# Performance work log

Measured on AMD Instinct MI355X. Metric: run time of the kernel, lower is better.

## Reference

```python
import jax, jax.numpy as jnp
import numpy as np

B, T, D, R = 4, 2048, 1024, 32


def setup_inputs() -> dict:
    key = jax.random.key(0)
    kx, ku = jax.random.split(key)
    x = jax.random.normal(kx, (B, T, D), dtype=jnp.float32)
    # low-rank metric factor; small init so distances are moderate
    U = jax.random.normal(ku, (D, R), dtype=jnp.float32) * 0.05
    return {"x": x, "U": U}


def reference(x, U):
    # g = U @ U.T (PSD low-rank metric).
    # dist_sq[b,t,j] = (x_t - x_j)^T g (x_t - x_j)
    #               = ||U^T x_t||^2 + ||U^T x_j||^2 - 2 (U^T x_t).(U^T x_j)
    # Algebraic expansion of the original O(B*T*T*D) broadcasted diff tensor.
    y = jnp.einsum('btd,dr->btr', x, U)                # [B,T,R]
    n = jnp.sum(y * y, axis=-1)                         # [B,T]
    cross = jnp.einsum('btr,bjr->btj', y, y)            # [B,T,T]
    dist_sq = n[:, :, None] + n[:, None, :] - 2.0 * cross
    attn = jax.nn.softmax(-dist_sq, axis=-1)            # [B,T,T]
    return jnp.einsum('btj,bjd->btd', attn, x)          # [B,T,D]
```

## Files before the change

### kernel.cpp

```cpp
#include <hip/hip_runtime.h>

#define B_ 4
#define T_ 2048
#define D_ 1024
#define R_ 32
#define XSTR 72

typedef __attribute__((ext_vector_type(8))) short short8;
typedef __attribute__((ext_vector_type(4))) float f32x4;
typedef __attribute__((ext_vector_type(4))) unsigned short us4;
typedef __attribute__((ext_vector_type(8))) unsigned short us8;

__device__ __forceinline__ unsigned short f2bf(float f) {
  union { float f; unsigned u; } v; v.f = f;
  unsigned r = (v.u + 0x7fffu + ((v.u >> 16) & 1u)) >> 16;
  return (unsigned short)r;
}
__device__ __forceinline__ float bf2f(unsigned short h) {
  union { unsigned u; float f; } v; v.u = (unsigned)h << 16;
  return v.f;
}

__global__ __launch_bounds__(256)
void geo_ut(const float* __restrict__ U, unsigned short* __restrict__ Ut) {
  __shared__ float tile[128][33];
  const int tid = threadIdx.x;
  const int d0 = blockIdx.x * 128;
  #pragma unroll
  for (int i = 0; i < 16; i++) {
    int e = i * 256 + tid;
    int d = e >> 5, r = e & 31;
    tile[d][r] = U[(size_t)(d0 + d) * R_ + r];
  }
  __syncthreads();
  const int r = tid >> 3, seg = tid & 7;
  us8 o0, o1;
  #pragma unroll
  for (int k = 0; k < 8; k++) o0[k] = f2bf(tile[seg * 16 + k][r]);
  #pragma unroll
  for (int k = 0; k < 8; k++) o1[k] = f2bf(tile[seg * 16 + 8 + k][r]);
  *(us8*)(Ut + (size_t)r * D_ + d0 + seg * 16) = o0;
  *(us8*)(Ut + (size_t)r * D_ + d0 + seg * 16 + 8) = o1;
}

__global__ __launch_bounds__(256)
void geo_prep(const float* __restrict__ x, const unsigned short* __restrict__ Ut,
              unsigned short* __restrict__ xt, unsigned short* __restrict__ ybf,
              float* __restrict__ nsq, float* __restrict__ l) {
  __shared__ unsigned short xs[32 * XSTR];
  __shared__ float ys[32][33];
  const int b = blockIdx.y;
  const int t0 = blockIdx.x * 32;
  const int tid = threadIdx.x, w = tid >> 6, lane = tid & 63;
  const int m = lane & 15, quad = lane >> 4;
  const int Mt = w & 1, Nt = w >> 1;
  const float* xb = x + ((size_t)b * T_ + t0) * D_;
  const int lr = tid >> 3;
  const int lc = (tid & 7) * 8;
  const int wd = tid >> 2;
  const int wt = (tid & 3) * 8;

  f32x4 acc = {0.f, 0.f, 0.f, 0.f};
  float4 r0 = *(const float4*)(xb + (size_t)lr * D_ + lc);
  float4 r1 = *(const float4*)(xb + (size_t)lr * D_ + lc + 4);

  for (int ch = 0; ch < 16; ch++) {
    const int d0 = ch * 64;
    us4 c0, c1;
    c0[0] = f2bf(r0.x); c0[1] = f2bf(r0.y); c0[2] = f2bf(r0.z); c0[3] = f2bf(r0.w);
    c1[0] = f2bf(r1.x); c1[1] = f2bf(r1.y); c1[2] = f2bf(r1.z); c1[3] = f2bf(r1.w);
    if (ch) __syncthreads();
    *(us4*)(xs + lr * XSTR + lc) = c0;
    *(us4*)(xs + lr * XSTR + lc + 4) = c1;
    if (ch + 1 < 16) {
      r0 = *(const float4*)(xb + (size_t)lr * D_ + d0 + 64 + lc);
      r1 = *(const float4*)(xb + (size_t)lr * D_ + d0 + 64 + lc + 4);
    }
    __syncthreads();
    us8 o;
    #pragma unroll
    for (int k = 0; k < 8; k++) o[k] = xs[(wt + k) * XSTR + wd];
    *(us8*)(xt + ((size_t)b * D_ + d0 + wd) * T_ + t0 + wt) = o;
    #pragma unroll
    for (int ks = 0; ks < 2; ks++) {
      short8 af = *(const short8*)(xs + (Mt * 16 + m) * XSTR + ks * 32 + quad * 8);
      short8 bf = *(const short8*)(Ut + (size_t)(Nt * 16 + m) * D_ + d0 + ks * 32 + quad * 8);
      acc = __builtin_amdgcn_mfma_f32_16x16x32_bf16(af, bf, acc, 0, 0, 0);
    }
  }
  #pragma unroll
  for (int r = 0; r < 4; r++)
    ys[Mt * 16 + quad * 4 + r][Nt * 16 + m] = acc[r];
  __syncthreads();
  {
    const int t = tid >> 3, rr = (tid & 7) * 4;
    us4 pk;
    #pragma unroll
    for (int r = 0; r < 4; r++) pk[r] = f2bf(1.41421356237f * ys[t][rr + r]);
    *(us4*)(ybf + ((size_t)b * T_ + t0 + t) * R_ + rr) = pk;
  }
  if (tid < 32) {
    float s = 0.f;
    #pragma unroll
    for (int r = 0; r < R_; r++) {
      float v = bf2f(f2bf(1.41421356237f * ys[tid][r]));
      s += v * v;
    }
    nsq[(size_t)b * T_ + t0 + tid] = 0.5f * s;
    l[(size_t)b * T_ + t0 + tid] = 0.f;
  }
}

__global__ __launch_bounds__(256)
void geo_scores(const unsigned short* __restrict__ ybf,
                const float* __restrict__ nsq,
                unsigned short* __restrict__ P, float* __restrict__ l,
                int jg0, int Kslab) {
  const int b = blockIdx.z;
  const int t0 = blockIdx.x * 128;
  const int jl0 = blockIdx.y * 128;
  const int tid = threadIdx.x, w = tid >> 6, lane = tid & 63;
  const int m = lane & 15, quad = lane >> 4;
  const unsigned short* yb = ybf + (size_t)b * T_ * R_;
  const float* nb = nsq + b * T_;
  const int jw = jl0 + w * 32;
  short8 aj[2]; f32x4 njv[2];
  #pragma unroll
  for (int rb = 0; rb < 2; rb++) {
    aj[rb] = *(const short8*)(yb + (size_t)(jg0 + jw + rb * 16 + m) * R_ + quad * 8);
    njv[rb] = *(const f32x4*)(nb + jg0 + jw + rb * 16 + quad * 4);
  }
  unsigned short* Pb = P + (size_t)b * T_ * Kslab;
  #pragma unroll 2
  for (int cb = 0; cb < 8; cb++) {
    const int t = t0 + cb * 16 + m;
    short8 bt = *(const short8*)(yb + (size_t)t * R_ + quad * 8);
    float nt = nb[t];
    float ls = 0.f;
    #pragma unroll
    for (int rb = 0; rb < 2; rb++) {
      f32x4 z = {0.f, 0.f, 0.f, 0.f};
      f32x4 c = __builtin_amdgcn_mfma_f32_16x16x32_bf16(aj[rb], bt, z, 0, 0, 0);
      us4 pk;
      #pragma unroll
      for (int r = 0; r < 4; r++) {
        float p = __expf(c[r] - njv[rb][r] - nt);
        ls += p;
        pk[r] = f2bf(p);
      }
      *(us4*)(Pb + (size_t)t * Kslab + jw + rb * 16 + quad * 4) = pk;
    }
    ls += __shfl_xor(ls, 16, 64);
    ls += __shfl_xor(ls, 32, 64);
    if (quad == 0) atomicAdd(&l[b * T_ + t], ls);
  }
}

__global__ __launch_bounds__(256)
void geo_pv(const unsigned short* __restrict__ P,
            const unsigned short* __restrict__ xt,
            const float* __restrict__ l, float* __restrict__ out,
            int Kslab, int kxt0, int accumulate, int normalize) {
  __shared__ unsigned short As[128 * 64];
  __shared__ unsigned short Bs[128 * 64];
  const int b = blockIdx.z;
  const int id = blockIdx.x;
  const int cls = id & 7, kk = id >> 3;
  const int t0 = (2 * cls + (kk >> 3)) * 128;
  const int d0 = (kk & 7) * 128;
  const int tid = threadIdx.x, w = tid >> 6, lane = tid & 63;
  const int m = lane & 15, quad = lane >> 4;
  const int wr = (w & 1) * 64, wc = (w >> 1) * 64;
  const int srow = lane >> 3, sslot = lane & 7;
  const unsigned short* Pb = P + ((size_t)b * T_ + t0) * Kslab;
  const unsigned short* Xb = xt + ((size_t)b * D_ + d0) * T_ + kxt0;
  f32x4 acc[4][4];
  #pragma unroll
  for (int i = 0; i < 4; i++)
    #pragma unroll
    for (int j = 0; j < 4; j++) acc[i][j] = (f32x4){0.f, 0.f, 0.f, 0.f};

  for (int k0 = 0; k0 < Kslab; k0 += 64) {
    __syncthreads();
    #pragma unroll
    for (int cc = 0; cc < 4; cc++) {
      const int row = w * 32 + cc * 8 + srow;
      const int gs = sslot ^ (row & 7);
      __builtin_amdgcn_global_load_lds(
          (const __attribute__((address_space(1))) void*)(Pb + (size_t)row * Kslab + k0 + gs * 8),
          (__attribute__((address_space(3))) void*)(As + (w * 32 + cc * 8) * 64),
          16, 0, 0);
      __builtin_amdgcn_global_load_lds(
          (const __attribute__((address_space(1))) void*)(Xb + (size_t)row * T_ + k0 + gs * 8),
          (__attribute__((address_space(3))) void*)(Bs + (w * 32 + cc * 8) * 64),
          16, 0, 0);
    }
    __syncthreads();
    #pragma unroll
    for (int ks = 0; ks < 2; ks++) {
      short8 af[4], bf[4];
      #pragma unroll
      for (int i = 0; i < 4; i++) {
        const int ra = wr + i * 16 + m;
        af[i] = *(const short8*)(As + ra * 64 + (((ks * 4 + quad) ^ (m & 7)) * 8));
        const int cd = wc + i * 16 + m;
        bf[i] = *(const short8*)(Bs + cd * 64 + (((ks * 4 + quad) ^ (m & 7)) * 8));
      }
      #pragma unroll
      for (int rb = 0; rb < 4; rb++)
        #pragma unroll
        for (int cb = 0; cb < 4; cb++)
          acc[rb][cb] = __builtin_amdgcn_mfma_f32_16x16x32_bf16(af[rb], bf[cb], acc[rb][cb], 0, 0, 0);
    }
  }
  float* ob = out + ((size_t)b * T_ + t0 + wr) * D_ + d0 + wc;
  #pragma unroll
  for (int rb = 0; rb < 4; rb++) {
    f32x4 lv = *(const f32x4*)(l + b * T_ + t0 + wr + rb * 16 + quad * 4);
    f32x4 inv;
    #pragma unroll
    for (int r = 0; r < 4; r++) inv[r] = 1.f / lv[r];
    #pragma unroll
    for (int cb = 0; cb < 4; cb++) {
      #pragma unroll
      for (int r = 0; r < 4; r++) {
        float* p = ob + (size_t)(rb * 16 + quad * 4 + r) * D_ + cb * 16 + m;
        float v = acc[rb][cb][r];
        if (accumulate) v += *p;
        if (normalize) v *= inv[r];
        *p = v;
      }
    }
  }
}

extern "C" void kernel_launch(void* const* d_in, const int* in_sizes, int n_in,
                              void* d_out, int out_size, void* d_ws, size_t ws_size,
                              hipStream_t stream) {
  const float* x = (const float*)d_in[0];
  const float* U = (const float*)d_in[1];
  float* out = (float*)d_out;

  const size_t xt_b  = (size_t)B_ * D_ * T_ * 2;
  const size_t ybf_b = (size_t)B_ * T_ * R_ * 2;
  const size_t nsq_b = (size_t)B_ * T_ * 4;
  const size_t l_b   = nsq_b;
  const size_t ut_b  = (size_t)D_ * R_ * 2;
  const size_t base  = xt_b + ybf_b + nsq_b + l_b + ut_b;
  const size_t pfull = (size_t)B_ * T_ * T_ * 2;

  int nslab = 16;
  const int cand[5] = {1, 2, 4, 8, 16};
  for (int i = 0; i < 5; i++)
    if (base + pfull / (size_t)cand[i] <= ws_size) { nslab = cand[i]; break; }
  const int Kslab = T_ / nslab;

  unsigned short* xtp = (unsigned short*)d_ws;
  unsigned short* ybf = (unsigned short*)((char*)d_ws + xt_b);
  float* nsq = (float*)((char*)d_ws + xt_b + ybf_b);
  float* lp  = (float*)((char*)d_ws + xt_b + ybf_b + nsq_b);
  unsigned short* Utp = (unsigned short*)((char*)d_ws + xt_b + ybf_b + nsq_b + l_b);
  unsigned short* P = (unsigned short*)((char*)d_ws + base);

  hipLaunchKernelGGL(geo_ut, dim3(D_ / 128), dim3(256), 0, stream, U, Utp);
  hipLaunchKernelGGL(geo_prep, dim3(T_ / 32, B_), dim3(256), 0, stream,
                     x, Utp, xtp, ybf, nsq, lp);
  for (int s = 0; s < nslab; s++) {
    hipLaunchKernelGGL(geo_scores, dim3(T_ / 128, Kslab / 128, B_), dim3(256), 0, stream,
                       ybf, nsq, P, lp, s * Kslab, Kslab);
    hipLaunchKernelGGL(geo_pv, dim3(128, 1, B_), dim3(256), 0, stream,
                       P, xtp, lp, out, Kslab, s * Kslab,
                       (int)(s > 0), (int)(s == nslab - 1));
  }
}
```

Before: 158.9 us.

## Split prep projection across D slabs with partial sums and separate reduce kernel

```diff
diff --git a/kernel.cpp b/kernel.cpp
--- a/kernel.cpp
+++ b/kernel.cpp
@@ -4,7 +4,7 @@
 #define T_ 2048
 #define D_ 1024
 #define R_ 32
-#define XSTR 72
+#define XSTR2 136
 
 typedef __attribute__((ext_vector_type(8))) short short8;
 typedef __attribute__((ext_vector_type(4))) float f32x4;
@@ -45,70 +45,89 @@
 
 __global__ __launch_bounds__(256)
 void geo_prep(const float* __restrict__ x, const unsigned short* __restrict__ Ut,
-              unsigned short* __restrict__ xt, unsigned short* __restrict__ ybf,
-              float* __restrict__ nsq, float* __restrict__ l) {
-  __shared__ unsigned short xs[32 * XSTR];
-  __shared__ float ys[32][33];
-  const int b = blockIdx.y;
+              unsigned short* __restrict__ xt, float* __restrict__ y_part) {
+  __shared__ unsigned short xs[2][32 * XSTR2];
+  const int b = blockIdx.y, slab = blockIdx.z;
   const int t0 = blockIdx.x * 32;
+  const int d0 = slab * 256;
   const int tid = threadIdx.x, w = tid >> 6, lane = tid & 63;
   const int m = lane & 15, quad = lane >> 4;
   const int Mt = w & 1, Nt = w >> 1;
-  const float* xb = x + ((size_t)b * T_ + t0) * D_;
   const int lr = tid >> 3;
-  const int lc = (tid & 7) * 8;
-  const int wd = tid >> 2;
-  const int wt = (tid & 3) * 8;
-
-  f32x4 acc = {0.f, 0.f, 0.f, 0.f};
-  float4 r0 = *(const float4*)(xb + (size_t)lr * D_ + lc);
-  float4 r1 = *(const float4*)(xb + (size_t)lr * D_ + lc + 4);
-
-  for (int ch = 0; ch < 16; ch++) {
-    const int d0 = ch * 64;
-    us4 c0, c1;
-    c0[0] = f2bf(r0.x); c0[1] = f2bf(r0.y); c0[2] = f2bf(r0.z); c0[3] = f2bf(r0.w);
-    c1[0] = f2bf(r1.x); c1[1] = f2bf(r1.y); c1[2] = f2bf(r1.z); c1[3] = f2bf(r1.w);
-    if (ch) __syncthreads();
-    *(us4*)(xs + lr * XSTR + lc) = c0;
-    *(us4*)(xs + lr * XSTR + lc + 4) = c1;
-    if (ch + 1 < 16) {
-      r0 = *(const float4*)(xb + (size_t)lr * D_ + d0 + 64 + lc);
-      r1 = *(const float4*)(xb + (size_t)lr * D_ + d0 + 64 + lc + 4);
-    }
-    __syncthreads();
-    us8 o;
-    #pragma unroll
-    for (int k = 0; k < 8; k++) o[k] = xs[(wt + k) * XSTR + wd];
-    *(us8*)(xt + ((size_t)b * D_ + d0 + wd) * T_ + t0 + wt) = o;
-    #pragma unroll
-    for (int ks = 0; ks < 2; ks++) {
-      short8 af = *(const short8*)(xs + (Mt * 16 + m) * XSTR + ks * 32 + quad * 8);
-      short8 bf = *(const short8*)(Ut + (size_t)(Nt * 16 + m) * D_ + d0 + ks * 32 + quad * 8);
-      acc = __builtin_amdgcn_mfma_f32_16x16x32_bf16(af, bf, acc, 0, 0, 0);
-    }
-  }
-  #pragma unroll
-  for (int r = 0; r < 4; r++)
-    ys[Mt * 16 + quad * 4 + r][Nt * 16 + m] = acc[r];
+  const int lc = (tid & 7) * 16;
+
+  const float* xb = x + ((size_t)b * T_ + t0 + lr) * D_ + d0 + lc;
+  float4 v[2][4];
+  #pragma unroll
+  for (int ch = 0; ch < 2; ch++)
+    #pragma unroll
+    for (int i = 0; i < 4; i++)
+      v[ch][i] = *(const float4*)(xb + ch * 128 + i * 4);
+  #pragma unroll
+  for (int ch = 0; ch < 2; ch++)
+    #pragma unroll
+    for (int i = 0; i < 4; i++) {
+      us4 c;
+      c[0] = f2bf(v[ch][i].x); c[1] = f2bf(v[ch][i].y);
+      c[2] = f2bf(v[ch][i].z); c[3] = f2bf(v[ch][i].w);
+      *(us4*)&xs[ch][lr * XSTR2 + lc + i * 4] = c;
+    }
   __syncthreads();
   {
-    const int t = tid >> 3, rr = (tid & 7) * 4;
-    us4 pk;
-    #pragma unroll
-    for (int r = 0; r < 4; r++) pk[r] = f2bf(1.41421356237f * ys[t][rr + r]);
-    *(us4*)(ybf + ((size_t)b * T_ + t0 + t) * R_ + rr) = pk;
-  }
-  if (tid < 32) {
-    float s = 0.f;
-    #pragma unroll
-    for (int r = 0; r < R_; r++) {
-      float v = bf2f(f2bf(1.41421356237f * ys[tid][r]));
-      s += v * v;
-    }
-    nsq[(size_t)b * T_ + t0 + tid] = 0.5f * s;
-    l[(size_t)b * T_ + t0 + tid] = 0.f;
-  }
+    const int wd = tid >> 1, wt = (tid & 1) * 16;
+    #pragma unroll
+    for (int ch = 0; ch < 2; ch++) {
+      us8 o0, o1;
+      #pragma unroll
+      for (int k = 0; k < 8; k++) {
+        o0[k] = xs[ch][(wt + k) * XSTR2 + wd];
+        o1[k] = xs[ch][(wt + 8 + k) * XSTR2 + wd];
+      }
+      unsigned short* xo = xt + ((size_t)b * D_ + d0 + ch * 128 + wd) * T_ + t0;
+      *(us8*)(xo + wt) = o0;
+      *(us8*)(xo + wt + 8) = o1;
+    }
+  }
+  f32x4 acc = {0.f, 0.f, 0.f, 0.f};
+  #pragma unroll
+  for (int ch = 0; ch < 2; ch++)
+    #pragma unroll
+    for (int ks = 0; ks < 4; ks++) {
+      short8 af = *(const short8*)&xs[ch][(Mt * 16 + m) * XSTR2 + ks * 32 + quad * 8];
+      short8 bf = *(const short8*)(Ut + (size_t)(Nt * 16 + m) * D_ + d0 + ch * 128 + ks * 32 + quad * 8);
+      acc = __builtin_amdgcn_mfma_f32_16x16x32_bf16(af, bf, acc, 0, 0, 0);
+    }
+  float* yp = y_part + ((size_t)(slab * B_ + b) * T_ + t0 + Mt * 16 + quad * 4) * R_ + Nt * 16 + m;
+  #pragma unroll
+  for (int k = 0; k < 4; k++) yp[(size_t)k * R_] = acc[k];
+}
+
+__global__ __launch_bounds__(256)
+void geo_reduce(const float* __restrict__ y_part, unsigned short* __restrict__ ybf,
+                float* __restrict__ nsq, float* __restrict__ l) {
+  const int tid = threadIdx.x;
+  const size_t row = (size_t)blockIdx.x * 32 + (tid >> 3);
+  const int r0 = (tid & 7) * 4;
+  f32x4 v = {0.f, 0.f, 0.f, 0.f};
+  #pragma unroll
+  for (int s = 0; s < 4; s++) {
+    f32x4 p = *(const f32x4*)(y_part + ((size_t)s * B_ * T_ + row) * R_ + r0);
+    #pragma unroll
+    for (int k = 0; k < 4; k++) v[k] += p[k];
+  }
+  us4 pk;
+  float part = 0.f;
+  #pragma unroll
+  for (int k = 0; k < 4; k++) {
+    pk[k] = f2bf(1.41421356237f * v[k]);
+    float b = bf2f(pk[k]);
+    part += b * b;
+  }
+  *(us4*)(ybf + row * R_ + r0) = pk;
+  part += __shfl_xor(part, 1, 64);
+  part += __shfl_xor(part, 2, 64);
+  part += __shfl_xor(part, 4, 64);
+  if ((tid & 7) == 0) { nsq[row] = 0.5f * part; l[row] = 0.f; }
 }
 
 __global__ __launch_bounds__(256)
@@ -131,11 +150,17 @@
     njv[rb] = *(const f32x4*)(nb + jg0 + jw + rb * 16 + quad * 4);
   }
   unsigned short* Pb = P + (size_t)b * T_ * Kslab;
+  short8 btn = *(const short8*)(yb + (size_t)(t0 + m) * R_ + quad * 8);
+  float ntn = nb[t0 + m];
   #pragma unroll 2
   for (int cb = 0; cb < 8; cb++) {
     const int t = t0 + cb * 16 + m;
-    short8 bt = *(const short8*)(yb + (size_t)t * R_ + quad * 8);
-    float nt = nb[t];
+    short8 bt = btn;
+    float nt = ntn;
+    if (cb < 7) {
+      btn = *(const short8*)(yb + (size_t)(t + 16) * R_ + quad * 8);
+      ntn = nb[t + 16];
+    }
     float ls = 0.f;
     #pragma unroll
     for (int rb = 0; rb < 2; rb++) {
@@ -246,7 +271,8 @@
   const size_t nsq_b = (size_t)B_ * T_ * 4;
   const size_t l_b   = nsq_b;
   const size_t ut_b  = (size_t)D_ * R_ * 2;
-  const size_t base  = xt_b + ybf_b + nsq_b + l_b + ut_b;
+  const size_t yp_b  = (size_t)4 * B_ * T_ * R_ * 4;
+  const size_t base  = xt_b + ybf_b + nsq_b + l_b + ut_b + yp_b;
   const size_t pfull = (size_t)B_ * T_ * T_ * 2;
 
   int nslab = 16;
@@ -255,16 +281,20 @@
     if (base + pfull / (size_t)cand[i] <= ws_size) { nslab = cand[i]; break; }
   const int Kslab = T_ / nslab;
 
-  unsigned short* xtp = (unsigned short*)d_ws;
-  unsigned short* ybf = (unsigned short*)((char*)d_ws + xt_b);
-  float* nsq = (float*)((char*)d_ws + xt_b + ybf_b);
-  float* lp  = (float*)((char*)d_ws + xt_b + ybf_b + nsq_b);
-  unsigned short* Utp = (unsigned short*)((char*)d_ws + xt_b + ybf_b + nsq_b + l_b);
-  unsigned short* P = (unsigned short*)((char*)d_ws + base);
+  char* wp = (char*)d_ws;
+  unsigned short* xtp = (unsigned short*)wp;                 wp += xt_b;
+  unsigned short* ybf = (unsigned short*)wp;                 wp += ybf_b;
+  float* nsq = (float*)wp;                                   wp += nsq_b;
+  float* lp  = (float*)wp;                                   wp += l_b;
+  unsigned short* Utp = (unsigned short*)wp;                 wp += ut_b;
+  float* ypart = (float*)wp;                                 wp += yp_b;
+  unsigned short* P = (unsigned short*)wp;
 
   hipLaunchKernelGGL(geo_ut, dim3(D_ / 128), dim3(256), 0, stream, U, Utp);
-  hipLaunchKernelGGL(geo_prep, dim3(T_ / 32, B_), dim3(256), 0, stream,
-                     x, Utp, xtp, ybf, nsq, lp);
+  hipLaunchKernelGGL(geo_prep, dim3(T_ / 32, B_, 4), dim3(256), 0, stream,
+                     x, Utp, xtp, ypart);
+  hipLaunchKernelGGL(geo_reduce, dim3(B_ * T_ / 32), dim3(256), 0, stream,
+                     ypart, ybf, nsq, lp);
   for (int s = 0; s < nslab; s++) {
     hipLaunchKernelGGL(geo_scores, dim3(T_ / 128, Kslab / 128, B_), dim3(256), 0, stream,
                        ybf, nsq, P, lp, s * Kslab, Kslab);
```

Result: faster. 155.6 us (-2.1%).
